# Kernel optimization log

Measured on AMD Instinct MI355X. Metric: run time of the kernel, lower is better.

Reference implementation:

```python
import jax, jax.numpy as jnp
import numpy as np


def setup_inputs() -> dict:
    key = jax.random.key(0)
    kq, kk, kv = jax.random.split(key, 3)
    B, H, SQ, KV, D = 2, 16, 2048, 4096, 128
    q = jax.random.normal(kq, (B, H, SQ, D), dtype=jnp.float32)
    k = jax.random.normal(kk, (B, H, KV, D), dtype=jnp.float32)
    v = jax.random.normal(kv, (B, H, KV, D), dtype=jnp.float32)
    return {"q": q, "k": k, "v": v}


def reference(q, k, v):
    # Faithful to F.scaled_dot_product_attention with a boolean mask that is
    # True for the first half of KV positions (masked positions -> -inf).
    KV = k.shape[2]
    D = q.shape[-1]
    scale = 1.0 / jnp.sqrt(jnp.asarray(D, dtype=q.dtype))
    # [B, H, Sq, KV] scores
    scores = jnp.einsum("bhqd,bhkd->bhqk", q, k) * scale
    kv_pos = jnp.arange(KV)
    mask = (kv_pos < KV // 2)[None, None, None, :]  # [1,1,1,KV]
    neg_inf = jnp.asarray(jnp.finfo(scores.dtype).min, dtype=scores.dtype)
    scores = jnp.where(mask, scores, neg_inf)
    attn = jax.nn.softmax(scores, axis=-1)
    return jnp.einsum("bhqk,bhkd->bhqd", attn, v)
```

## Files before the change

kernel.cpp:

```cpp
#include <hip/hip_runtime.h>


#define NT 32
#define LDK 136
#define LDP 72

typedef _Float16 half8  __attribute__((ext_vector_type(8)));
typedef __fp16   fp16x2 __attribute__((ext_vector_type(2)));
typedef float    floatx4 __attribute__((ext_vector_type(4)));
typedef unsigned int uint;

#if __has_builtin(__builtin_amdgcn_exp2f)
#define EXP2(x) __builtin_amdgcn_exp2f(x)
#else
#define EXP2(x) exp2f(x)
#endif

union H2U { fp16x2 h; uint u; };
union H8U { uint u[4]; half8 h; };

static __device__ __forceinline__ uint pk(float a, float b) {
    H2U z; z.h = __builtin_amdgcn_cvt_pkrtz(a, b); return z.u;
}

__global__ __launch_bounds__(512, 2)
void fa_kernel(const float* __restrict__ Q, const float* __restrict__ K,
               const float* __restrict__ V, float* __restrict__ O) {
    const float SCALE = 0.08838834764831845f * 1.4426950408889634f;

    __shared__ _Float16 kbuf[2][64 * LDK];
    __shared__ _Float16 vbuf[2][128 * 64];
    __shared__ _Float16 pbuf[256 * LDP];

    const int t    = threadIdx.x;
    const int lane = t & 63;
    const int w    = t >> 6;
    const int wq   = w & 3;
    const int h    = w >> 2;
    const int c    = lane & 15;
    const int qd   = lane >> 4;

    const int idx  = blockIdx.x;
    const int xcd  = idx & 7;
    const int slot = idx >> 3;
    const int qt   = slot & 7;
    const int bh   = xcd + 8 * (slot >> 3);
    const int q0   = qt * 256;

    const float* Qb = Q + (size_t)bh * 2048 * 128;
    const float* Kb = K + (size_t)bh * 4096 * 128;
    const float* Vb = V + (size_t)bh * 4096 * 128;
    float*       Ob = O + (size_t)bh * 2048 * 128;

    half8 bq[4][4];
    #pragma unroll
    for (int m = 0; m < 4; ++m) {
        #pragma unroll
        for (int s = 0; s < 4; ++s) {
            const int row = q0 + 64 * wq + 16 * m + c;
            const int col = 32 * s + 8 * qd;
            floatx4 x = *(const floatx4*)(Qb + (size_t)row * 128 + col);
            floatx4 y = *(const floatx4*)(Qb + (size_t)row * 128 + col + 4);
            H8U hh;
            hh.u[0] = pk(x[0] * SCALE, x[1] * SCALE);
            hh.u[1] = pk(x[2] * SCALE, x[3] * SCALE);
            hh.u[2] = pk(y[0] * SCALE, y[1] * SCALE);
            hh.u[3] = pk(y[2] * SCALE, y[3] * SCALE);
            bq[m][s] = hh.h;
        }
    }

    floatx4 o[4][4];
    float lsum[4] = {0.f, 0.f, 0.f, 0.f};
    #pragma unroll
    for (int a = 0; a < 4; ++a)
        #pragma unroll
        for (int b = 0; b < 4; ++b) o[a][b] = (floatx4){0.f, 0.f, 0.f, 0.f};

    const int krw = t >> 4;
    const int kd0 = 8 * (t & 15);
    const int vp  = (t >> 3) & 31;
    const int vd0 = 8 * ((t & 7) | ((t >> 8) << 3));

    floatx4 kpre[2][2], vpre[2][2];

    #define LOAD_TILE(kv0)                                                          \
        {   const int _b = (kv0);                                                   \
            _Pragma("unroll")                                                       \
            for (int i = 0; i < 2; ++i) {                                           \
                const float* p = Kb + (size_t)(_b + krw + 32 * i) * 128 + kd0;      \
                kpre[i][0] = *(const floatx4*)p;                                    \
                kpre[i][1] = *(const floatx4*)(p + 4);                              \
            }                                                                       \
            _Pragma("unroll")                                                       \
            for (int r = 0; r < 2; ++r) {                                           \
                const float* p = Vb + (size_t)(_b + 2 * vp + r) * 128 + vd0;        \
                vpre[r][0] = *(const floatx4*)p;                                    \
                vpre[r][1] = *(const floatx4*)(p + 4);                              \
            } }

    #define STAGE_TILE(buf)                                                         \
        {   const int _s = (buf);                                                   \
            _Pragma("unroll")                                                       \
            for (int i = 0; i < 2; ++i) {                                           \
                H8U hh;                                                             \
                hh.u[0] = pk(kpre[i][0][0], kpre[i][0][1]);                         \
                hh.u[1] = pk(kpre[i][0][2], kpre[i][0][3]);                         \
                hh.u[2] = pk(kpre[i][1][0], kpre[i][1][1]);                         \
                hh.u[3] = pk(kpre[i][1][2], kpre[i][1][3]);                         \
                *(half8*)&kbuf[_s][(krw + 32 * i) * LDK + kd0] = hh.h;              \
            }                                                                       \
            _Pragma("unroll")                                                       \
            for (int e = 0; e < 8; ++e) {                                           \
                const int d   = vd0 + e;                                            \
                const int rot = 8 * ((d >> 1) & 7);                                 \
                const int qq  = (2 * vp + rot) & 63;                                \
                *(uint*)&vbuf[_s][d * 64 + qq] =                                    \
                    pk(vpre[0][e >> 2][e & 3], vpre[1][e >> 2][e & 3]);             \
            } }

    LOAD_TILE(0);
    STAGE_TILE(0);
    __syncthreads();

    for (int kt = 0; kt < NT; ++kt) {
        const int cur = kt & 1;

        if (kt + 1 < NT) LOAD_TILE((kt + 1) * 64);

        floatx4 st[2][4];
        #pragma unroll
        for (int ntl = 0; ntl < 2; ++ntl)
            #pragma unroll
            for (int m = 0; m < 4; ++m) st[ntl][m] = (floatx4){0.f, 0.f, 0.f, 0.f};
        #pragma unroll
        for (int ntl = 0; ntl < 2; ++ntl) {
            #pragma unroll
            for (int s = 0; s < 4; ++s) {
                half8 ka = *(const half8*)&kbuf[cur][(32 * h + 16 * ntl + c) * LDK + 32 * s + 8 * qd];
                #pragma unroll
                for (int m = 0; m < 4; ++m)
                    st[ntl][m] = __builtin_amdgcn_mfma_f32_16x16x32_f16(ka, bq[m][s], st[ntl][m], 0, 0, 0);
            }
        }

        #pragma unroll
        for (int ntl = 0; ntl < 2; ++ntl) {
            #pragma unroll
            for (int m = 0; m < 4; ++m) {
                const float p0 = EXP2(st[ntl][m][0]);
                const float p1 = EXP2(st[ntl][m][1]);
                const float p2 = EXP2(st[ntl][m][2]);
                const float p3 = EXP2(st[ntl][m][3]);
                lsum[m] += (p0 + p1) + (p2 + p3);
                uint2 pr;
                pr.x = pk(p0, p1);
                pr.y = pk(p2, p3);
                *(uint2*)&pbuf[(64 * wq + 16 * m + c) * LDP + 32 * h + 16 * ntl + 4 * qd] = pr;
            }
        }
        __syncthreads();

        half8 pb[2][4];
        #pragma unroll
        for (int kb = 0; kb < 2; ++kb)
            #pragma unroll
            for (int m = 0; m < 4; ++m)
                pb[kb][m] = *(const half8*)&pbuf[(64 * wq + 16 * m + c) * LDP + 32 * kb + 8 * qd];

        #pragma unroll
        for (int mtd = 0; mtd < 4; ++mtd) {
            const int d = 64 * h + 16 * mtd + c;
            #pragma unroll
            for (int kb = 0; kb < 2; ++kb) {
                const int base = (32 * kb + 8 * qd + 8 * ((d >> 1) & 7)) & 63;
                half8 va = *(const half8*)&vbuf[cur][d * 64 + base];
                #pragma unroll
                for (int m = 0; m < 4; ++m)
                    o[m][mtd] = __builtin_amdgcn_mfma_f32_16x16x32_f16(va, pb[kb][m], o[m][mtd], 0, 0, 0);
            }
        }

        if (kt + 1 < NT) STAGE_TILE(1 - cur);
        __syncthreads();
    }

    #pragma unroll
    for (int m = 0; m < 4; ++m) {
        lsum[m] += __shfl_xor(lsum[m], 16, 64);
        lsum[m] += __shfl_xor(lsum[m], 32, 64);
    }
    float* lbuf = (float*)pbuf;
    if (qd == 0) {
        #pragma unroll
        for (int m = 0; m < 4; ++m)
            lbuf[h * 256 + 64 * wq + 16 * m + c] = lsum[m];
    }
    __syncthreads();

    #pragma unroll
    for (int m = 0; m < 4; ++m) {
        const int qrow = 64 * wq + 16 * m + c;
        const float invl = 1.0f / (lbuf[qrow] + lbuf[256 + qrow]);
        #pragma unroll
        for (int mtd = 0; mtd < 4; ++mtd) {
            floatx4 r = o[m][mtd];
            r[0] *= invl; r[1] *= invl; r[2] *= invl; r[3] *= invl;
            *(floatx4*)&Ob[(size_t)(q0 + qrow) * 128 + 64 * h + 16 * mtd + 4 * qd] = r;
        }
    }
}

extern "C" void kernel_launch(void* const* d_in, const int* in_sizes, int n_in,
                              void* d_out, int out_size, void* d_ws, size_t ws_size,
                              hipStream_t stream) {
    const float* q = (const float*)d_in[0];
    const float* k = (const float*)d_in[1];
    const float* v = (const float*)d_in[2];
    float* out = (float*)d_out;
    fa_kernel<<<dim3(256), dim3(512), 0, stream>>>(q, k, v, out);
}
```

Baseline: 250.3 us.

## Pre-convert K/V to fp16 in workspace and stream tiles via global_load_lds

Adds a preprocessing kernel that converts the unmasked first half of K to fp16 with an XOR-swizzled layout and transposes V into fp16, both written to the workspace. The attention kernel then loads these tiles straight into LDS with async global_load_lds instead of loading fp32 into registers and converting per block. It also halves the query tile per block to 128 rows, doubling the grid to 512 blocks with a higher occupancy hint, and single-buffers K. The goal is to cut redundant fp32 K/V reads and conversion work that every query block repeated, at the cost of an extra kernel launch and a workspace round-trip.

```diff
diff --git a/kernel.cpp b/kernel.cpp
--- a/kernel.cpp
+++ b/kernel.cpp
@@ -1,8 +1,7 @@
 #include <hip/hip_runtime.h>
 
 
-#define NT 32
-#define LDK 136
+#define NT  32
 #define LDP 72
 
 typedef _Float16 half8  __attribute__((ext_vector_type(8)));
@@ -23,14 +22,77 @@
     H2U z; z.h = __builtin_amdgcn_cvt_pkrtz(a, b); return z.u;
 }
 
-__global__ __launch_bounds__(512, 2)
-void fa_kernel(const float* __restrict__ Q, const float* __restrict__ K,
-               const float* __restrict__ V, float* __restrict__ O) {
+#define KH_BH 524288u
+#define VT_BASE 16777216u
+#define VT_BH 524288u
+
+#define GLOAD_LDS16(g, l)                                                     \
+    __builtin_amdgcn_global_load_lds(                                         \
+        (const __attribute__((address_space(1))) uint*)(const void*)(g),      \
+        (__attribute__((address_space(3))) uint*)(void*)(l), 16, 0, 0)
+
+__global__ __launch_bounds__(256)
+void cvt_kernel(const float* __restrict__ K, const float* __restrict__ V,
+                char* __restrict__ ws) {
+    const int bid = blockIdx.x;
+    const int bh  = bid >> 5;
+    const int kv0 = (bid & 31) * 64;
+    const int t   = threadIdx.x;
+
+    const float* Kb = K + (size_t)bh * 4096 * 128 + (size_t)kv0 * 128;
+    const float* Vb = V + (size_t)bh * 4096 * 128 + (size_t)kv0 * 128;
+    char* Khb = ws + (size_t)bh * KH_BH + (size_t)kv0 * 256;
+    char* Vtb = ws + VT_BASE + (size_t)bh * VT_BH;
+
+    __shared__ _Float16 vb[128 * 72];
+
+    {
+        const int r  = t >> 2;
+        const int xb = (t & 3) * 4;
+        const float* src = Kb + r * 128 + xb * 8;
+        #pragma unroll
+        for (int x = 0; x < 4; ++x) {
+            floatx4 a = *(const floatx4*)(src + 8 * x);
+            floatx4 b = *(const floatx4*)(src + 8 * x + 4);
+            H8U h;
+            h.u[0] = pk(a[0], a[1]); h.u[1] = pk(a[2], a[3]);
+            h.u[2] = pk(b[0], b[1]); h.u[3] = pk(b[2], b[3]);
+            *(half8*)(Khb + r * 256 + 16 * ((xb + x) ^ (r & 7))) = h.h;
+        }
+    }
+    {
+        const int kv = 2 * (t >> 3);
+        const int d0 = (t & 7) * 16;
+        #pragma unroll
+        for (int g = 0; g < 4; ++g) {
+            floatx4 a = *(const floatx4*)(Vb + (size_t)kv * 128 + d0 + 4 * g);
+            floatx4 b = *(const floatx4*)(Vb + (size_t)(kv + 1) * 128 + d0 + 4 * g);
+            #pragma unroll
+            for (int e = 0; e < 4; ++e)
+                *(uint*)&vb[(d0 + 4 * g + e) * 72 + kv] = pk(a[e], b[e]);
+        }
+    }
+    __syncthreads();
+    {
+        const int d  = t >> 1;
+        const int yg = t & 1;
+        #pragma unroll
+        for (int y4 = 0; y4 < 4; ++y4) {
+            const int y = 4 * yg + y4;
+            half8 h = *(const half8*)&vb[d * 72 + 8 * y];
+            *(half8*)(Vtb + (size_t)d * 4096 + (size_t)kv0 * 2 + 16 * (y ^ (d & 7))) = h;
+        }
+    }
+}
+
+__global__ __launch_bounds__(512, 4)
+void fa_kernel(const float* __restrict__ Q, float* __restrict__ O,
+               const char* __restrict__ ws) {
     const float SCALE = 0.08838834764831845f * 1.4426950408889634f;
 
-    __shared__ _Float16 kbuf[2][64 * LDK];
+    __shared__ _Float16 kbuf[64 * 128];
     __shared__ _Float16 vbuf[2][128 * 64];
-    __shared__ _Float16 pbuf[256 * LDP];
+    __shared__ _Float16 pbuf[128 * LDP];
 
     const int t    = threadIdx.x;
     const int lane = t & 63;
@@ -39,28 +101,29 @@
     const int h    = w >> 2;
     const int c    = lane & 15;
     const int qd   = lane >> 4;
+    const int ck   = c & 7;
 
     const int idx  = blockIdx.x;
     const int xcd  = idx & 7;
     const int slot = idx >> 3;
-    const int qt   = slot & 7;
-    const int bh   = xcd + 8 * (slot >> 3);
-    const int q0   = qt * 256;
-
-    const float* Qb = Q + (size_t)bh * 2048 * 128;
-    const float* Kb = K + (size_t)bh * 4096 * 128;
-    const float* Vb = V + (size_t)bh * 4096 * 128;
-    float*       Ob = O + (size_t)bh * 2048 * 128;
-
-    half8 bq[4][4];
-    #pragma unroll
-    for (int m = 0; m < 4; ++m) {
+    const int qt   = slot & 15;
+    const int bh   = xcd + 8 * (slot >> 4);
+    const int q0   = qt * 128;
+
+    const float* Qb  = Q + (size_t)bh * 2048 * 128;
+    float*       Ob  = O + (size_t)bh * 2048 * 128;
+    const char*  Khb = ws + (size_t)bh * KH_BH;
+    const char*  Vtb = ws + VT_BASE + (size_t)bh * VT_BH;
+
+    half8 bq[2][4];
+    #pragma unroll
+    for (int m = 0; m < 2; ++m) {
         #pragma unroll
         for (int s = 0; s < 4; ++s) {
-            const int row = q0 + 64 * wq + 16 * m + c;
-            const int col = 32 * s + 8 * qd;
-            floatx4 x = *(const floatx4*)(Qb + (size_t)row * 128 + col);
-            floatx4 y = *(const floatx4*)(Qb + (size_t)row * 128 + col + 4);
+            const int row = q0 + 32 * wq + 16 * m + c;
+            const float* p = Qb + (size_t)row * 128 + 32 * s + 8 * qd;
+            floatx4 x = *(const floatx4*)p;
+            floatx4 y = *(const floatx4*)(p + 4);
             H8U hh;
             hh.u[0] = pk(x[0] * SCALE, x[1] * SCALE);
             hh.u[1] = pk(x[2] * SCALE, x[3] * SCALE);
@@ -70,76 +133,49 @@
         }
     }
 
-    floatx4 o[4][4];
-    float lsum[4] = {0.f, 0.f, 0.f, 0.f};
-    #pragma unroll
-    for (int a = 0; a < 4; ++a)
+    floatx4 o[2][4];
+    float lsum[2] = {0.f, 0.f};
+    #pragma unroll
+    for (int a = 0; a < 2; ++a)
         #pragma unroll
         for (int b = 0; b < 4; ++b) o[a][b] = (floatx4){0.f, 0.f, 0.f, 0.f};
 
-    const int krw = t >> 4;
-    const int kd0 = 8 * (t & 15);
-    const int vp  = (t >> 3) & 31;
-    const int vd0 = 8 * ((t & 7) | ((t >> 8) << 3));
-
-    floatx4 kpre[2][2], vpre[2][2];
-
-    #define LOAD_TILE(kv0)                                                          \
-        {   const int _b = (kv0);                                                   \
-            _Pragma("unroll")                                                       \
-            for (int i = 0; i < 2; ++i) {                                           \
-                const float* p = Kb + (size_t)(_b + krw + 32 * i) * 128 + kd0;      \
-                kpre[i][0] = *(const floatx4*)p;                                    \
-                kpre[i][1] = *(const floatx4*)(p + 4);                              \
-            }                                                                       \
-            _Pragma("unroll")                                                       \
-            for (int r = 0; r < 2; ++r) {                                           \
-                const float* p = Vb + (size_t)(_b + 2 * vp + r) * 128 + vd0;        \
-                vpre[r][0] = *(const floatx4*)p;                                    \
-                vpre[r][1] = *(const floatx4*)(p + 4);                              \
-            } }
-
-    #define STAGE_TILE(buf)                                                         \
-        {   const int _s = (buf);                                                   \
-            _Pragma("unroll")                                                       \
-            for (int i = 0; i < 2; ++i) {                                           \
-                H8U hh;                                                             \
-                hh.u[0] = pk(kpre[i][0][0], kpre[i][0][1]);                         \
-                hh.u[1] = pk(kpre[i][0][2], kpre[i][0][3]);                         \
-                hh.u[2] = pk(kpre[i][1][0], kpre[i][1][1]);                         \
-                hh.u[3] = pk(kpre[i][1][2], kpre[i][1][3]);                         \
-                *(half8*)&kbuf[_s][(krw + 32 * i) * LDK + kd0] = hh.h;              \
-            }                                                                       \
-            _Pragma("unroll")                                                       \
-            for (int e = 0; e < 8; ++e) {                                           \
-                const int d   = vd0 + e;                                            \
-                const int rot = 8 * ((d >> 1) & 7);                                 \
-                const int qq  = (2 * vp + rot) & 63;                                \
-                *(uint*)&vbuf[_s][d * 64 + qq] =                                    \
-                    pk(vpre[0][e >> 2][e & 3], vpre[1][e >> 2][e & 3]);             \
-            } }
-
-    LOAD_TILE(0);
-    STAGE_TILE(0);
+    #define ISSUE_K(kv0_)                                                          \
+        { _Pragma("unroll")                                                        \
+          for (int j = 0; j < 2; ++j) {                                            \
+              const int i = 2 * w + j;                                             \
+              const char* g = Khb + (size_t)(kv0_) * 256 +                         \
+                              (size_t)(4 * i + (lane >> 4)) * 256 + (lane & 15) * 16; \
+              GLOAD_LDS16(g, (char*)kbuf + i * 1024); } }
+    #define ISSUE_V(kv0_, buf_)                                                    \
+        { _Pragma("unroll")                                                        \
+          for (int j = 0; j < 2; ++j) {                                            \
+              const int i = 2 * w + j;                                             \
+              const char* g = Vtb + (size_t)(8 * i + (lane >> 3)) * 4096 +         \
+                              (size_t)(kv0_) * 2 + (lane & 7) * 16;                \
+              GLOAD_LDS16(g, (char*)vbuf[buf_] + i * 1024); } }
+
+    ISSUE_K(0);
+    ISSUE_V(0, 0);
     __syncthreads();
 
     for (int kt = 0; kt < NT; ++kt) {
         const int cur = kt & 1;
-
-        if (kt + 1 < NT) LOAD_TILE((kt + 1) * 64);
-
-        floatx4 st[2][4];
+        if (kt + 1 < NT) ISSUE_V((kt + 1) * 64, 1 - cur);
+
+        floatx4 st[2][2];
         #pragma unroll
         for (int ntl = 0; ntl < 2; ++ntl)
             #pragma unroll
-            for (int m = 0; m < 4; ++m) st[ntl][m] = (floatx4){0.f, 0.f, 0.f, 0.f};
+            for (int m = 0; m < 2; ++m) st[ntl][m] = (floatx4){0.f, 0.f, 0.f, 0.f};
         #pragma unroll
         for (int ntl = 0; ntl < 2; ++ntl) {
+            const int r = 32 * h + 16 * ntl + c;
             #pragma unroll
             for (int s = 0; s < 4; ++s) {
-                half8 ka = *(const half8*)&kbuf[cur][(32 * h + 16 * ntl + c) * LDK + 32 * s + 8 * qd];
+                half8 ka = *(const half8*)((const char*)kbuf + r * 256 + 16 * ((4 * s + qd) ^ ck));
                 #pragma unroll
-                for (int m = 0; m < 4; ++m)
+                for (int m = 0; m < 2; ++m)
                     st[ntl][m] = __builtin_amdgcn_mfma_f32_16x16x32_f16(ka, bq[m][s], st[ntl][m], 0, 0, 0);
             }
         }
@@ -147,61 +183,58 @@
         #pragma unroll
         for (int ntl = 0; ntl < 2; ++ntl) {
             #pragma unroll
-            for (int m = 0; m < 4; ++m) {
+            for (int m = 0; m < 2; ++m) {
                 const float p0 = EXP2(st[ntl][m][0]);
                 const float p1 = EXP2(st[ntl][m][1]);
                 const float p2 = EXP2(st[ntl][m][2]);
                 const float p3 = EXP2(st[ntl][m][3]);
                 lsum[m] += (p0 + p1) + (p2 + p3);
-                uint2 pr;
-                pr.x = pk(p0, p1);
-                pr.y = pk(p2, p3);
-                *(uint2*)&pbuf[(64 * wq + 16 * m + c) * LDP + 32 * h + 16 * ntl + 4 * qd] = pr;
+                uint2 pr; pr.x = pk(p0, p1); pr.y = pk(p2, p3);
+                *(uint2*)&pbuf[(32 * wq + 16 * m + c) * LDP + 32 * h + 16 * ntl + 4 * qd] = pr;
             }
         }
         __syncthreads();
 
-        half8 pb[2][4];
+        if (kt + 1 < NT) ISSUE_K((kt + 1) * 64);
+
+        half8 pb[2][2];
         #pragma unroll
         for (int kb = 0; kb < 2; ++kb)
             #pragma unroll
-            for (int m = 0; m < 4; ++m)
-                pb[kb][m] = *(const half8*)&pbuf[(64 * wq + 16 * m + c) * LDP + 32 * kb + 8 * qd];
+            for (int m = 0; m < 2; ++m)
+                pb[kb][m] = *(const half8*)&pbuf[(32 * wq + 16 * m + c) * LDP + 32 * kb + 8 * qd];
 
         #pragma unroll
         for (int mtd = 0; mtd < 4; ++mtd) {
             const int d = 64 * h + 16 * mtd + c;
             #pragma unroll
             for (int kb = 0; kb < 2; ++kb) {
-                const int base = (32 * kb + 8 * qd + 8 * ((d >> 1) & 7)) & 63;
-                half8 va = *(const half8*)&vbuf[cur][d * 64 + base];
+                half8 va = *(const half8*)((const char*)vbuf[cur] + d * 128 + 16 * ((4 * kb + qd) ^ ck));
                 #pragma unroll
-                for (int m = 0; m < 4; ++m)
+                for (int m = 0; m < 2; ++m)
                     o[m][mtd] = __builtin_amdgcn_mfma_f32_16x16x32_f16(va, pb[kb][m], o[m][mtd], 0, 0, 0);
             }
         }
-
-        if (kt + 1 < NT) STAGE_TILE(1 - cur);
         __syncthreads();
     }
 
     #pragma unroll
-    for (int m = 0; m < 4; ++m) {
+    for (int m = 0; m < 2; ++m) {
         lsum[m] += __shfl_xor(lsum[m], 16, 64);
         lsum[m] += __shfl_xor(lsum[m], 32, 64);
     }
     float* lbuf = (float*)pbuf;
     if (qd == 0) {
         #pragma unroll
-        for (int m = 0; m < 4; ++m)
-            lbuf[h * 256 + 64 * wq + 16 * m + c] = lsum[m];
+        for (int m = 0; m < 2; ++m)
+            lbuf[h * 128 + 32 * wq + 16 * m + c] = lsum[m];
     }
     __syncthreads();
 
     #pragma unroll
-    for (int m = 0; m < 4; ++m) {
-        const int qrow = 64 * wq + 16 * m + c;
-        const float invl = 1.0f / (lbuf[qrow] + lbuf[256 + qrow]);
+    for (int m = 0; m < 2; ++m) {
+        const int qrow = 32 * wq + 16 * m + c;
+        const float invl = 1.0f / (lbuf[qrow] + lbuf[128 + qrow]);
         #pragma unroll
         for (int mtd = 0; mtd < 4; ++mtd) {
             floatx4 r = o[m][mtd];
@@ -218,5 +251,7 @@
     const float* k = (const float*)d_in[1];
     const float* v = (const float*)d_in[2];
     float* out = (float*)d_out;
-    fa_kernel<<<dim3(256), dim3(512), 0, stream>>>(q, k, v, out);
-}
+    char* ws = (char*)d_ws;
+    cvt_kernel<<<dim3(1024), dim3(256), 0, stream>>>(k, v, ws);
+    fa_kernel<<<dim3(512), dim3(512), 0, stream>>>(q, out, ws);
+}
```

Result: faster. 237.2 us (-5.2%).
